# Kernel optimization log

Measured on AMD Instinct MI355X. Metric: run time of the kernel, lower is better.

Reference implementation:

```python
import math
import jax, jax.numpy as jnp
import numpy as np

T, D, H = 2048, 1024, 16
DH = D // H
DFF = 4 * D
EPS = 1e-5


def gelu(x):
    c = math.sqrt(2.0 / math.pi)
    return 0.5 * x * (1.0 + jnp.tanh(c * (x + 0.044715 * jnp.power(x, 3))))


def layer_norm(x, w, b):
    mu = jnp.mean(x, axis=-1, keepdims=True)
    var = jnp.var(x, axis=-1, keepdims=True)
    return (x - mu) / jnp.sqrt(var + EPS) * w + b


def setup_inputs() -> dict:
    key = jax.random.key(0)
    ks = jax.random.split(key, 8)
    s = lambda fan_in: 1.0 / math.sqrt(fan_in)
    return {
        "x": jax.random.normal(ks[0], (T, D), jnp.float32),
        "w_kqv": jax.random.uniform(ks[1], (3 * D, D), jnp.float32, -s(D), s(D)),
        "b_kqv": jnp.zeros((3 * D,), jnp.float32),
        "w_o": jax.random.uniform(ks[2], (D, D), jnp.float32, -s(D), s(D)),
        "b_o": jnp.zeros((D,), jnp.float32),
        "ln1_w": jnp.ones((D,), jnp.float32),
        "ln1_b": jnp.zeros((D,), jnp.float32),
        "ln2_w": jnp.ones((D,), jnp.float32),
        "ln2_b": jnp.zeros((D,), jnp.float32),
        "w_up": jax.random.uniform(ks[3], (DFF, D), jnp.float32, -s(D), s(D)),
        "b_up": jnp.zeros((DFF,), jnp.float32),
        "w_down": jax.random.uniform(ks[4], (D, DFF), jnp.float32, -s(DFF), s(DFF)),
        "b_down": jnp.zeros((D,), jnp.float32),
    }


def _block(x, w_kqv, b_kqv, w_o, b_o, ln1_w, ln1_b, ln2_w, ln2_b,
           w_up, b_up, w_down, b_down):
    t = x.shape[0]
    # --- causal attention ---
    h = layer_norm(x, ln1_w, ln1_b)
    kqv = h @ w_kqv.T + b_kqv                      # [t, 3D]
    k, q, v = jnp.split(kqv, 3, axis=-1)
    # rearrange 't (d h) -> h t d' : head index is the FAST axis (as in source)
    to_heads = lambda m: m.reshape(t, DH, H).transpose(2, 0, 1)  # [H, t, DH]
    k, q, v = to_heads(k), to_heads(q), to_heads(v)
    # NOTE: source divides by sqrt(1/d) == multiplies by sqrt(d_head)
    logits = jnp.einsum('hqd,hkd->hqk', q, k) * math.sqrt(DH)
    mask = jnp.tril(jnp.ones((t, t), dtype=bool))
    logits = jnp.where(mask, logits, -jnp.inf)
    attn_w = jax.nn.softmax(logits, axis=-1)       # [H, t, t]
    hv = jnp.einsum('hqK,hKd->hqd', attn_w, v)     # [H, t, DH]
    # rearrange 'h q d -> q (h d)' : head index is the SLOW axis (as in source)
    hv = hv.transpose(1, 0, 2).reshape(t, D)
    x = x + (hv @ w_o.T + b_o)
    # --- MLP ---
    h2 = layer_norm(x, ln2_w, ln2_b)
    z = gelu(h2 @ w_up.T + b_up) @ w_down.T + b_down
    return x + z


def reference(x, w_kqv, b_kqv, w_o, b_o, ln1_w, ln1_b, ln2_w, ln2_b,
              w_up, b_up, w_down, b_down):
    return _block(x, w_kqv, b_kqv, w_o, b_o, ln1_w, ln1_b, ln2_w, ln2_b,
                  w_up, b_up, w_down, b_down)
```

## Files before the change

### kernel.cpp

```cpp
#include <hip/hip_runtime.h>
#include <math.h>

#define TT 2048
#define DD 1024
#define NH 16
#define DHD 64
#define DFF 4096

typedef __attribute__((ext_vector_type(8))) short short8;
typedef __attribute__((ext_vector_type(4))) float f32x4;

#define MFMA16(a, b, c) __builtin_amdgcn_mfma_f32_16x16x32_bf16(a, b, c, 0, 0, 0)
#define GLDS16(gp, lp) __builtin_amdgcn_global_load_lds( \
    (const __attribute__((address_space(1))) void*)(gp), \
    (__attribute__((address_space(3))) void*)(lp), 16, 0, 0)

static __device__ __forceinline__ unsigned short f2b(float f) {
  unsigned u = __builtin_bit_cast(unsigned, f);
  u = u + 0x7fffu + ((u >> 16) & 1u);
  return (unsigned short)(u >> 16);
}
static __device__ __forceinline__ float b2f(unsigned short b) {
  return __builtin_bit_cast(float, (unsigned)b << 16);
}

__global__ __launch_bounds__(256) void f2b4_kernel(const float* __restrict__ s0,
    const float* __restrict__ s1, const float* __restrict__ s2,
    const float* __restrict__ s3, unsigned short* __restrict__ out) {
  int i = blockIdx.x * 256 + threadIdx.x;
  const float* s; int off;
  if (i < 786432)       { s = s0; off = 0; }
  else if (i < 1048576) { s = s1; off = 786432; }
  else if (i < 2097152) { s = s2; off = 1048576; }
  else                  { s = s3; off = 2097152; }
  float4 v = ((const float4*)s)[i - off];
  ushort4 o;
  o.x = f2b(v.x); o.y = f2b(v.y); o.z = f2b(v.z); o.w = f2b(v.w);
  ((ushort4*)out)[i] = o;
}

__global__ __launch_bounds__(256) void ln_kernel(const float* __restrict__ x,
    const float* __restrict__ w, const float* __restrict__ b,
    unsigned short* __restrict__ out) {
  int row = blockIdx.x;
  const float4* xr = (const float4*)(x + (size_t)row * DD);
  float4 v = xr[threadIdx.x];
  float s  = v.x + v.y + v.z + v.w;
  float ss = v.x * v.x + v.y * v.y + v.z * v.z + v.w * v.w;
  for (int o = 32; o > 0; o >>= 1) {
    s  += __shfl_down(s, o);
    ss += __shfl_down(ss, o);
  }
  __shared__ float red[10];
  int lane = threadIdx.x & 63, wv = threadIdx.x >> 6;
  if (lane == 0) { red[wv] = s; red[4 + wv] = ss; }
  __syncthreads();
  if (threadIdx.x == 0) {
    float S  = red[0] + red[1] + red[2] + red[3];
    float SS = red[4] + red[5] + red[6] + red[7];
    float mu  = S * (1.0f / DD);
    float var = SS * (1.0f / DD) - mu * mu;
    red[8] = mu;
    red[9] = rsqrtf(var + 1e-5f);
  }
  __syncthreads();
  float mu = red[8], inv = red[9];
  float4 wv4 = ((const float4*)w)[threadIdx.x];
  float4 bv4 = ((const float4*)b)[threadIdx.x];
  ushort4 o4;
  o4.x = f2b((v.x - mu) * inv * wv4.x + bv4.x);
  o4.y = f2b((v.y - mu) * inv * wv4.y + bv4.y);
  o4.z = f2b((v.z - mu) * inv * wv4.z + bv4.z);
  o4.w = f2b((v.w - mu) * inv * wv4.w + bv4.w);
  ((ushort4*)(out + (size_t)row * DD))[threadIdx.x] = o4;
}

template<int FUSE_GELU, int OUT_BF16, int HAS_RESID, int PARTIAL>
__global__ __launch_bounds__(256) void gemm3(
    const unsigned short* __restrict__ A,
    const unsigned short* __restrict__ Bw,
    const float* __restrict__ bias,
    const float* __restrict__ resid,
    void* __restrict__ Cout,
    int M, int N, int K, int KS) {
  __shared__ char lds[65536];
  const int tid = threadIdx.x;
  const int w = tid >> 6, l = tid & 63;
  const int l15 = l & 15, lhi = l >> 4;
  const int row0 = blockIdx.y * 128, col0 = blockIdx.x * 128;
  const int kbeg = blockIdx.z * KS;
  const int wm = (w >> 1) * 64, wn = (w & 1) * 64;

  f32x4 acc[4][4] = {};

  const int slotp = (l & 7) ^ (l >> 3);
  const int srow = w * 32 + 2 * (l >> 3) + (slotp >> 2);
  const int scolb = (slotp & 3) * 16;
  const char* aS = (const char*)A + ((size_t)(row0 + srow) * K + kbeg) * 2 + scolb;
  const char* bS = (const char*)Bw + ((size_t)(col0 + srow) * K + kbeg) * 2 + scolb;
  const size_t r16 = (size_t)K * 32;
  const int aLo = w * 2048;
  const int bLo = 8192 + w * 2048;

  int aOff[4], bOff[4];
#pragma unroll
  for (int i = 0; i < 4; ++i) {
    int ra = wm + i * 16 + l15;
    aOff[i] = (ra >> 1) * 128 + (((( ra & 1) << 6) | (lhi << 4)) ^ (((ra >> 1) & 7) << 4));
    int rb = wn + i * 16 + l15;
    bOff[i] = 8192 + (rb >> 1) * 128 + ((((rb & 1) << 6) | (lhi << 4)) ^ (((rb >> 1) & 7) << 4));
  }

  const int NT = KS >> 5;

  auto STAGE = [&](int t) {
    char* base = lds + (t & 3) * 16384;
    const char* a = aS + (size_t)t * 64;
    const char* b = bS + (size_t)t * 64;
    GLDS16(a, base + aLo);
    GLDS16(a + r16, base + aLo + 1024);
    GLDS16(b, base + bLo);
    GLDS16(b + r16, base + bLo + 1024);
  };
  auto COMPUTE = [&](int t) {
    const char* buf = lds + (t & 3) * 16384;
    short8 af[4], bf[4];
#pragma unroll
    for (int mi = 0; mi < 4; ++mi) af[mi] = *(const short8*)(buf + aOff[mi]);
#pragma unroll
    for (int ni = 0; ni < 4; ++ni) bf[ni] = *(const short8*)(buf + bOff[ni]);
#pragma unroll
    for (int mi = 0; mi < 4; ++mi)
#pragma unroll
      for (int ni = 0; ni < 4; ++ni)
        acc[mi][ni] = MFMA16(af[mi], bf[ni], acc[mi][ni]);
  };

  STAGE(0); STAGE(1); STAGE(2);

  int t = 0;
  for (; t < NT - 2; ++t) {
    __builtin_amdgcn_sched_barrier(0);
    asm volatile("s_waitcnt vmcnt(8)" ::: "memory");
    __builtin_amdgcn_s_barrier();
    __builtin_amdgcn_sched_barrier(0);
    if (t + 3 < NT) STAGE(t + 3);
    COMPUTE(t);
  }
  __builtin_amdgcn_sched_barrier(0);
  asm volatile("s_waitcnt vmcnt(4)" ::: "memory");
  __builtin_amdgcn_s_barrier();
  __builtin_amdgcn_sched_barrier(0);
  COMPUTE(NT - 2);
  __builtin_amdgcn_sched_barrier(0);
  asm volatile("s_waitcnt vmcnt(0)" ::: "memory");
  __builtin_amdgcn_s_barrier();
  __builtin_amdgcn_sched_barrier(0);
  COMPUTE(NT - 1);

  if (PARTIAL) {
    unsigned short* Cp = (unsigned short*)Cout + (size_t)blockIdx.z * M * N;
#pragma unroll
    for (int mi = 0; mi < 4; ++mi)
#pragma unroll
      for (int r = 0; r < 4; ++r) {
        size_t row = (size_t)(row0 + wm + mi * 16 + lhi * 4 + r);
#pragma unroll
        for (int ni = 0; ni < 4; ++ni)
          Cp[row * N + col0 + wn + ni * 16 + l15] = f2b(acc[mi][ni][r]);
      }
    return;
  }

#pragma unroll
  for (int mi = 0; mi < 4; ++mi) {
#pragma unroll
    for (int r = 0; r < 4; ++r) {
      size_t row = (size_t)(row0 + wm + mi * 16 + lhi * 4 + r);
#pragma unroll
      for (int ni = 0; ni < 4; ++ni) {
        int col = col0 + wn + ni * 16 + l15;
        float v = acc[mi][ni][r] + bias[col];
        if (FUSE_GELU) {
          float u = v;
          v = 0.5f * u * (1.0f + tanhf(0.7978845608028654f * (u + 0.044715f * u * u * u)));
        }
        if (HAS_RESID) v += resid[row * N + col];
        if (OUT_BF16) ((unsigned short*)Cout)[row * N + col] = f2b(v);
        else          ((float*)Cout)[row * N + col] = v;
      }
    }
  }
}

template<int NP>
__global__ __launch_bounds__(256) void reduce_k(const unsigned short* __restrict__ p,
    const float* __restrict__ bias, const float* __restrict__ resid,
    float* __restrict__ out) {
  int i = blockIdx.x * 256 + threadIdx.x;
  float4 r = ((const float4*)resid)[i];
  float4 bb = ((const float4*)bias)[i & (DD / 4 - 1)];
  float o0 = r.x + bb.x, o1 = r.y + bb.y, o2 = r.z + bb.z, o3 = r.w + bb.w;
#pragma unroll
  for (int z = 0; z < NP; ++z) {
    ushort4 pv = ((const ushort4*)(p + (size_t)z * TT * DD))[i];
    o0 += b2f(pv.x); o1 += b2f(pv.y); o2 += b2f(pv.z); o3 += b2f(pv.w);
  }
  float4 o; o.x = o0; o.y = o1; o.z = o2; o.w = o3;
  ((float4*)out)[i] = o;
}

__global__ __launch_bounds__(256) void gather_qkv(const unsigned short* __restrict__ kqv,
    unsigned short* __restrict__ Q, unsigned short* __restrict__ K) {
  int idx = blockIdx.x * 256 + threadIdx.x;
  int d = idx & 63;
  int t = (idx >> 6) & (TT - 1);
  int h = idx >> 17;
  int col = d * NH + h;
  const unsigned short* rowp = kqv + (size_t)t * (3 * DD);
  K[idx] = rowp[col];
  Q[idx] = f2b(b2f(rowp[DD + col]) * 8.0f);
}

__global__ __launch_bounds__(256) void transpose_v(const unsigned short* __restrict__ kqv,
    unsigned short* __restrict__ Vt) {
  const int h = blockIdx.y;
  const int t0 = blockIdx.x * 64;
  __shared__ unsigned short Vs[64][65];
  for (int idx = threadIdx.x; idx < 4096; idx += 256) {
    int t = idx >> 6, d = idx & 63;
    Vs[t][d] = kqv[(size_t)(t0 + t) * (3 * DD) + 2 * DD + d * NH + h];
  }
  __syncthreads();
  for (int idx = threadIdx.x; idx < 4096; idx += 256) {
    int d = idx >> 6, t = idx & 63;
    Vt[(size_t)(h * DHD + d) * TT + t0 + t] = Vs[t][d];
  }
}

__global__ __launch_bounds__(256) void attn_mfma(
    const unsigned short* __restrict__ Q,
    const unsigned short* __restrict__ K,
    const unsigned short* __restrict__ Vt,
    unsigned short* __restrict__ hv) {
  const int h = blockIdx.y;
  const int qb = gridDim.x - 1 - blockIdx.x;
  const int q0 = qb * 64;
  const int tid = threadIdx.x;
  const int w = tid >> 6, l = tid & 63;
  const int l15 = l & 15, lhi = l >> 4;

  __shared__ char lds[40960];
  char* Ps = lds + 32768 + w * 2048;

  const char* KhB = (const char*)(K + (size_t)h * TT * DHD);
  const char* VhB = (const char*)(Vt + (size_t)h * DHD * TT);

  const unsigned short* Qbase = Q + ((size_t)h * TT + q0 + w * 16 + l15) * DHD;
  short8 qf0 = *(const short8*)(Qbase + lhi * 8);
  short8 qf1 = *(const short8*)(Qbase + 32 + lhi * 8);

  f32x4 oacc[4] = {};
  float m = -1e30f, lsum = 0.0f;

  const int lrow = l >> 3;
  const int colb = ((l & 7) * 16) ^ (lrow << 4);
  const int srow = w * 16 + lrow;
  const int swz = (l15 & 7) << 4;

  auto stage = [&](int k0n, char* buf) {
    const char* ks = KhB + (size_t)(k0n + srow) * 128 + colb;
    GLDS16(ks, buf + w * 2048);
    GLDS16(ks + 8 * 128, buf + w * 2048 + 1024);
    const char* vs = VhB + (size_t)srow * (TT * 2) + (size_t)k0n * 2 + colb;
    GLDS16(vs, buf + 8192 + w * 2048);
    GLDS16(vs + 8 * (TT * 2), buf + 8192 + w * 2048 + 1024);
  };

  stage(0, lds);
  __syncthreads();
  int cur = 0;

  for (int kt = 0; kt <= qb; ++kt) {
    if (kt < qb) stage((kt + 1) * 64, lds + (cur ^ 1) * 16384);

    const char* Kb = lds + cur * 16384;
    const char* Vb = Kb + 8192;

    f32x4 sacc[4] = {};
    __builtin_amdgcn_s_setprio(1);
#pragma unroll
    for (int nt = 0; nt < 4; ++nt) {
      const char* rp = Kb + (nt * 16 + l15) * 128;
      short8 kb0 = *(const short8*)(rp + ((lhi * 16) ^ swz));
      short8 kb1 = *(const short8*)(rp + ((64 + lhi * 16) ^ swz));
      sacc[nt] = MFMA16(kb0, qf0, sacc[nt]);
      sacc[nt] = MFMA16(kb1, qf1, sacc[nt]);
    }
    __builtin_amdgcn_s_setprio(0);

    if (kt == qb) {
      const int qloc = w * 16 + l15;
#pragma unroll
      for (int nt = 0; nt < 4; ++nt)
#pragma unroll
        for (int r = 0; r < 4; ++r)
          if (nt * 16 + lhi * 4 + r > qloc) sacc[nt][r] = -1e30f;
    }

    float tmax = -1e30f;
#pragma unroll
    for (int nt = 0; nt < 4; ++nt)
#pragma unroll
      for (int r = 0; r < 4; ++r) tmax = fmaxf(tmax, sacc[nt][r]);
    tmax = fmaxf(tmax, __shfl_xor(tmax, 16));
    tmax = fmaxf(tmax, __shfl_xor(tmax, 32));
    float mnew = fmaxf(m, tmax);
    float al = __expf(m - mnew);
    m = mnew;
    float ssum = 0.0f;
#pragma unroll
    for (int nt = 0; nt < 4; ++nt)
#pragma unroll
      for (int r = 0; r < 4; ++r) {
        float p = __expf(sacc[nt][r] - mnew);
        sacc[nt][r] = p;
        ssum += p;
      }
    ssum += __shfl_xor(ssum, 16);
    ssum += __shfl_xor(ssum, 32);
    lsum = lsum * al + ssum;

    {
      char* pp = Ps + l15 * 128;
#pragma unroll
      for (int nt = 0; nt < 4; ++nt) {
        uint2 pk;
        pk.x = (unsigned)f2b(sacc[nt][0]) | ((unsigned)f2b(sacc[nt][1]) << 16);
        pk.y = (unsigned)f2b(sacc[nt][2]) | ((unsigned)f2b(sacc[nt][3]) << 16);
        *(uint2*)(pp + (((nt * 16 + lhi * 4) * 2) ^ swz)) = pk;
      }
    }

    float alr[4];
#pragma unroll
    for (int r = 0; r < 4; ++r) alr[r] = __shfl(al, (l & 48) | (lhi * 4 + r));
#pragma unroll
    for (int dt = 0; dt < 4; ++dt)
#pragma unroll
      for (int r = 0; r < 4; ++r) oacc[dt][r] *= alr[r];

    const char* pr = Ps + l15 * 128;
    short8 pa0 = *(const short8*)(pr + ((lhi * 16) ^ swz));
    short8 pa1 = *(const short8*)(pr + ((64 + lhi * 16) ^ swz));
    __builtin_amdgcn_s_setprio(1);
#pragma unroll
    for (int dt = 0; dt < 4; ++dt) {
      const char* vr = Vb + (dt * 16 + l15) * 128;
      short8 vb0 = *(const short8*)(vr + ((lhi * 16) ^ swz));
      short8 vb1 = *(const short8*)(vr + ((64 + lhi * 16) ^ swz));
      oacc[dt] = MFMA16(pa0, vb0, oacc[dt]);
      oacc[dt] = MFMA16(pa1, vb1, oacc[dt]);
    }
    __builtin_amdgcn_s_setprio(0);

    __syncthreads();
    cur ^= 1;
  }

  float lr[4];
#pragma unroll
  for (int r = 0; r < 4; ++r)
    lr[r] = 1.0f / __shfl(lsum, (l & 48) | (lhi * 4 + r));
#pragma unroll
  for (int r = 0; r < 4; ++r) {
    size_t orow = (size_t)(q0 + w * 16 + lhi * 4 + r) * DD + h * 64;
#pragma unroll
    for (int dt = 0; dt < 4; ++dt)
      hv[orow + dt * 16 + l15] = f2b(oacc[dt][r] * lr[r]);
  }
}

extern "C" void kernel_launch(void* const* d_in, const int* in_sizes, int n_in,
                              void* d_out, int out_size, void* d_ws, size_t ws_size,
                              hipStream_t stream) {
  const float* x     = (const float*)d_in[0];
  const float* w_kqv = (const float*)d_in[1];
  const float* b_kqv = (const float*)d_in[2];
  const float* w_o   = (const float*)d_in[3];
  const float* b_o   = (const float*)d_in[4];
  const float* ln1_w = (const float*)d_in[5];
  const float* ln1_b = (const float*)d_in[6];
  const float* ln2_w = (const float*)d_in[7];
  const float* ln2_b = (const float*)d_in[8];
  const float* w_up  = (const float*)d_in[9];
  const float* b_up  = (const float*)d_in[10];
  const float* w_dn  = (const float*)d_in[11];
  const float* b_dn  = (const float*)d_in[12];
  float* out = (float*)d_out;

  char* W = (char*)d_ws;
  unsigned short* wkqv_b = (unsigned short*)(W);
  unsigned short* wo_b   = (unsigned short*)(W + 6291456);
  unsigned short* wup_b  = (unsigned short*)(W + 8388608);
  unsigned short* wdn_b  = (unsigned short*)(W + 16777216);
  unsigned short* h_b    = (unsigned short*)(W + 25165824);
  unsigned short* kqz    = (unsigned short*)(W + 29360128);
  unsigned short* Qg     = (unsigned short*)(W + 46137344);
  unsigned short* Kg     = (unsigned short*)(W + 50331648);
  unsigned short* Vtg    = (unsigned short*)(W + 54525952);
  unsigned short* hv_b   = (unsigned short*)(W + 58720256);
  float*          x2     = (float*)(W + 62914560);
  unsigned short* pproj  = (unsigned short*)(W + 29360128);
  unsigned short* pdown  = (unsigned short*)(W + 46137344);

  f2b4_kernel<<<3145728 / 256, 256, 0, stream>>>(w_kqv, w_o, w_up, w_dn, wkqv_b);

  ln_kernel<<<TT, 256, 0, stream>>>(x, ln1_w, ln1_b, h_b);
  gemm3<0, 1, 0, 0><<<dim3(3 * DD / 128, TT / 128, 1), 256, 0, stream>>>(
      h_b, wkqv_b, b_kqv, nullptr, kqz, TT, 3 * DD, DD, DD);
  gather_qkv<<<(NH * TT * DHD) / 256, 256, 0, stream>>>(kqz, Qg, Kg);
  transpose_v<<<dim3(TT / 64, NH), 256, 0, stream>>>(kqz, Vtg);
  attn_mfma<<<dim3(TT / 64, NH), 256, 0, stream>>>(Qg, Kg, Vtg, hv_b);
  gemm3<0, 0, 0, 1><<<dim3(DD / 128, TT / 128, 2), 256, 0, stream>>>(
      hv_b, wo_b, nullptr, nullptr, pproj, TT, DD, DD, DD / 2);
  reduce_k<2><<<TT * DD / 4 / 256, 256, 0, stream>>>(pproj, b_o, x, x2);
  ln_kernel<<<TT, 256, 0, stream>>>(x2, ln2_w, ln2_b, h_b);
  gemm3<1, 1, 0, 0><<<dim3(DFF / 128, TT / 128, 1), 256, 0, stream>>>(
      h_b, wup_b, b_up, nullptr, kqz, TT, DFF, DD, DD);
  gemm3<0, 0, 0, 1><<<dim3(DD / 128, TT / 128, 4), 256, 0, stream>>>(
      kqz, wdn_b, nullptr, nullptr, pdown, TT, DD, DFF, DFF / 4);
  reduce_k<4><<<TT * DD / 4 / 256, 256, 0, stream>>>(pdown, b_dn, x2, out);
}
```

Baseline: 184.4 us.

## Remap GEMM and attention blocks per XCD and switch GEMM to BK=64 double buffering

GEMM blocks now come from a 1D grid and are remapped so that each of the 8 XCDs gets a contiguous CX×CY patch of output tiles, so blocks on the same XCD share A/B rows in L2. The GEMM K-step grows from 32 to 64 with two 32 KB LDS buffers instead of four 16 KB ones, using a simpler row-swizzled layout. The attention grid is likewise remapped so each XCD handles two heads, and its initial __syncthreads is replaced with explicit vmcnt waits plus barriers. Pipeline depth drops from three stages in flight to one prefetch, which may expose more load latency.

```diff
diff --git a/kernel.cpp b/kernel.cpp
--- a/kernel.cpp
+++ b/kernel.cpp
@@ -76,90 +76,88 @@
 }
 
 template<int FUSE_GELU, int OUT_BF16, int HAS_RESID, int PARTIAL>
-__global__ __launch_bounds__(256) void gemm3(
+__global__ __launch_bounds__(256) void gemm4(
     const unsigned short* __restrict__ A,
     const unsigned short* __restrict__ Bw,
     const float* __restrict__ bias,
     const float* __restrict__ resid,
     void* __restrict__ Cout,
-    int M, int N, int K, int KS) {
+    int M, int N, int K, int KS, int CX, int CY) {
   __shared__ char lds[65536];
   const int tid = threadIdx.x;
   const int w = tid >> 6, l = tid & 63;
   const int l15 = l & 15, lhi = l >> 4;
-  const int row0 = blockIdx.y * 128, col0 = blockIdx.x * 128;
-  const int kbeg = blockIdx.z * KS;
+
+  const int GX = N >> 7, GYM = M >> 7;
+  const int xcd = blockIdx.x & 7, s = blockIdx.x >> 3;
+  const int ncx = GX / CX;
+  const int bx = (xcd % ncx) * CX + (s % CX);
+  const int yz = (xcd / ncx) * CY + (s / CX);
+  const int by = yz % GYM, bz = yz / GYM;
+
+  const int row0 = by << 7, col0 = bx << 7;
+  const int kbeg = bz * KS;
   const int wm = (w >> 1) * 64, wn = (w & 1) * 64;
 
   f32x4 acc[4][4] = {};
 
-  const int slotp = (l & 7) ^ (l >> 3);
-  const int srow = w * 32 + 2 * (l >> 3) + (slotp >> 2);
-  const int scolb = (slotp & 3) * 16;
-  const char* aS = (const char*)A + ((size_t)(row0 + srow) * K + kbeg) * 2 + scolb;
-  const char* bS = (const char*)Bw + ((size_t)(col0 + srow) * K + kbeg) * 2 + scolb;
-  const size_t r16 = (size_t)K * 32;
-  const int aLo = w * 2048;
-  const int bLo = 8192 + w * 2048;
-
-  int aOff[4], bOff[4];
-#pragma unroll
-  for (int i = 0; i < 4; ++i) {
-    int ra = wm + i * 16 + l15;
-    aOff[i] = (ra >> 1) * 128 + (((( ra & 1) << 6) | (lhi << 4)) ^ (((ra >> 1) & 7) << 4));
-    int rb = wn + i * 16 + l15;
-    bOff[i] = 8192 + (rb >> 1) * 128 + ((((rb & 1) << 6) | (lhi << 4)) ^ (((rb >> 1) & 7) << 4));
-  }
-
-  const int NT = KS >> 5;
+  const int lr = l >> 3;
+  const int cb = ((l & 7) * 16) ^ (lr << 4);
+  const char* aS = (const char*)A + ((size_t)(row0 + w * 32 + lr) * K + kbeg) * 2 + cb;
+  const char* bS = (const char*)Bw + ((size_t)(col0 + w * 32 + lr) * K + kbeg) * 2 + cb;
+  const size_t r8 = (size_t)K * 16;
+  const int aO = w * 4096, bO = 16384 + w * 4096;
+  const int NT = KS >> 6;
 
   auto STAGE = [&](int t) {
-    char* base = lds + (t & 3) * 16384;
-    const char* a = aS + (size_t)t * 64;
-    const char* b = bS + (size_t)t * 64;
-    GLDS16(a, base + aLo);
-    GLDS16(a + r16, base + aLo + 1024);
-    GLDS16(b, base + bLo);
-    GLDS16(b + r16, base + bLo + 1024);
+    char* base = lds + (t & 1) * 32768;
+    const char* a = aS + (size_t)t * 128;
+    const char* b = bS + (size_t)t * 128;
+    GLDS16(a,            base + aO);
+    GLDS16(a +     r8,   base + aO + 1024);
+    GLDS16(a + 2 * r8,   base + aO + 2048);
+    GLDS16(a + 3 * r8,   base + aO + 3072);
+    GLDS16(b,            base + bO);
+    GLDS16(b +     r8,   base + bO + 1024);
+    GLDS16(b + 2 * r8,   base + bO + 2048);
+    GLDS16(b + 3 * r8,   base + bO + 3072);
   };
   auto COMPUTE = [&](int t) {
-    const char* buf = lds + (t & 3) * 16384;
-    short8 af[4], bf[4];
-#pragma unroll
-    for (int mi = 0; mi < 4; ++mi) af[mi] = *(const short8*)(buf + aOff[mi]);
-#pragma unroll
-    for (int ni = 0; ni < 4; ++ni) bf[ni] = *(const short8*)(buf + bOff[ni]);
-#pragma unroll
-    for (int mi = 0; mi < 4; ++mi)
+    const char* Ab = lds + (t & 1) * 32768;
+    const char* Bb = Ab + 16384;
+    const int sw = (l15 & 7) << 4;
+#pragma unroll
+    for (int kk = 0; kk < 2; ++kk) {
+      short8 af[4], bf[4];
+#pragma unroll
+      for (int mi = 0; mi < 4; ++mi)
+        af[mi] = *(const short8*)(Ab + (wm + mi * 16 + l15) * 128 + ((kk * 64 + lhi * 16) ^ sw));
 #pragma unroll
       for (int ni = 0; ni < 4; ++ni)
-        acc[mi][ni] = MFMA16(af[mi], bf[ni], acc[mi][ni]);
+        bf[ni] = *(const short8*)(Bb + (wn + ni * 16 + l15) * 128 + ((kk * 64 + lhi * 16) ^ sw));
+#pragma unroll
+      for (int mi = 0; mi < 4; ++mi)
+#pragma unroll
+        for (int ni = 0; ni < 4; ++ni)
+          acc[mi][ni] = MFMA16(af[mi], bf[ni], acc[mi][ni]);
+    }
   };
 
-  STAGE(0); STAGE(1); STAGE(2);
-
-  int t = 0;
-  for (; t < NT - 2; ++t) {
-    __builtin_amdgcn_sched_barrier(0);
-    asm volatile("s_waitcnt vmcnt(8)" ::: "memory");
+  STAGE(0);
+  for (int t = 0; t < NT; ++t) {
+    if (t + 1 < NT) STAGE(t + 1);
+    __builtin_amdgcn_sched_barrier(0);
+    if (t + 1 < NT) asm volatile("s_waitcnt vmcnt(8)" ::: "memory");
+    else            asm volatile("s_waitcnt vmcnt(0)" ::: "memory");
     __builtin_amdgcn_s_barrier();
     __builtin_amdgcn_sched_barrier(0);
-    if (t + 3 < NT) STAGE(t + 3);
     COMPUTE(t);
-  }
-  __builtin_amdgcn_sched_barrier(0);
-  asm volatile("s_waitcnt vmcnt(4)" ::: "memory");
-  __builtin_amdgcn_s_barrier();
-  __builtin_amdgcn_sched_barrier(0);
-  COMPUTE(NT - 2);
-  __builtin_amdgcn_sched_barrier(0);
-  asm volatile("s_waitcnt vmcnt(0)" ::: "memory");
-  __builtin_amdgcn_s_barrier();
-  __builtin_amdgcn_sched_barrier(0);
-  COMPUTE(NT - 1);
+    __builtin_amdgcn_sched_barrier(0);
+    __builtin_amdgcn_s_barrier();
+  }
 
   if (PARTIAL) {
-    unsigned short* Cp = (unsigned short*)Cout + (size_t)blockIdx.z * M * N;
+    unsigned short* Cp = (unsigned short*)Cout + (size_t)bz * M * N;
 #pragma unroll
     for (int mi = 0; mi < 4; ++mi)
 #pragma unroll
@@ -243,8 +241,10 @@
     const unsigned short* __restrict__ K,
     const unsigned short* __restrict__ Vt,
     unsigned short* __restrict__ hv) {
-  const int h = blockIdx.y;
-  const int qb = gridDim.x - 1 - blockIdx.x;
+  const int bid = blockIdx.x;
+  const int xcd = bid & 7, s = bid >> 3;
+  const int qb = 31 - (s & 31);
+  const int h  = xcd * 2 + (s >> 5);
   const int q0 = qb * 64;
   const int tid = threadIdx.x;
   const int w = tid >> 6, l = tid & 63;
@@ -263,9 +263,9 @@
   f32x4 oacc[4] = {};
   float m = -1e30f, lsum = 0.0f;
 
-  const int lrow = l >> 3;
-  const int colb = ((l & 7) * 16) ^ (lrow << 4);
-  const int srow = w * 16 + lrow;
+  const int lr = l >> 3;
+  const int colb = ((l & 7) * 16) ^ (lr << 4);
+  const int srow = w * 16 + lr;
   const int swz = (l15 & 7) << 4;
 
   auto stage = [&](int k0n, char* buf) {
@@ -278,11 +278,15 @@
   };
 
   stage(0, lds);
-  __syncthreads();
   int cur = 0;
 
   for (int kt = 0; kt <= qb; ++kt) {
     if (kt < qb) stage((kt + 1) * 64, lds + (cur ^ 1) * 16384);
+    __builtin_amdgcn_sched_barrier(0);
+    if (kt < qb) asm volatile("s_waitcnt vmcnt(4)" ::: "memory");
+    else         asm volatile("s_waitcnt vmcnt(0)" ::: "memory");
+    __builtin_amdgcn_s_barrier();
+    __builtin_amdgcn_sched_barrier(0);
 
     const char* Kb = lds + cur * 16384;
     const char* Vb = Kb + 8192;
@@ -364,20 +368,21 @@
     }
     __builtin_amdgcn_s_setprio(0);
 
-    __syncthreads();
+    __builtin_amdgcn_sched_barrier(0);
+    __builtin_amdgcn_s_barrier();
     cur ^= 1;
   }
 
-  float lr[4];
+  float lr4[4];
 #pragma unroll
   for (int r = 0; r < 4; ++r)
-    lr[r] = 1.0f / __shfl(lsum, (l & 48) | (lhi * 4 + r));
+    lr4[r] = 1.0f / __shfl(lsum, (l & 48) | (lhi * 4 + r));
 #pragma unroll
   for (int r = 0; r < 4; ++r) {
     size_t orow = (size_t)(q0 + w * 16 + lhi * 4 + r) * DD + h * 64;
 #pragma unroll
     for (int dt = 0; dt < 4; ++dt)
-      hv[orow + dt * 16 + l15] = f2b(oacc[dt][r] * lr[r]);
+      hv[orow + dt * 16 + l15] = f2b(oacc[dt][r] * lr4[r]);
   }
 }
 
@@ -417,18 +422,18 @@
   f2b4_kernel<<<3145728 / 256, 256, 0, stream>>>(w_kqv, w_o, w_up, w_dn, wkqv_b);
 
   ln_kernel<<<TT, 256, 0, stream>>>(x, ln1_w, ln1_b, h_b);
-  gemm3<0, 1, 0, 0><<<dim3(3 * DD / 128, TT / 128, 1), 256, 0, stream>>>(
-      h_b, wkqv_b, b_kqv, nullptr, kqz, TT, 3 * DD, DD, DD);
+  gemm4<0, 1, 0, 0><<<384, 256, 0, stream>>>(
+      h_b, wkqv_b, b_kqv, nullptr, kqz, TT, 3 * DD, DD, DD, 6, 8);
   gather_qkv<<<(NH * TT * DHD) / 256, 256, 0, stream>>>(kqz, Qg, Kg);
   transpose_v<<<dim3(TT / 64, NH), 256, 0, stream>>>(kqz, Vtg);
-  attn_mfma<<<dim3(TT / 64, NH), 256, 0, stream>>>(Qg, Kg, Vtg, hv_b);
-  gemm3<0, 0, 0, 1><<<dim3(DD / 128, TT / 128, 2), 256, 0, stream>>>(
-      hv_b, wo_b, nullptr, nullptr, pproj, TT, DD, DD, DD / 2);
+  attn_mfma<<<512, 256, 0, stream>>>(Qg, Kg, Vtg, hv_b);
+  gemm4<0, 0, 0, 1><<<256, 256, 0, stream>>>(
+      hv_b, wo_b, nullptr, nullptr, pproj, TT, DD, DD, DD / 2, 8, 4);
   reduce_k<2><<<TT * DD / 4 / 256, 256, 0, stream>>>(pproj, b_o, x, x2);
   ln_kernel<<<TT, 256, 0, stream>>>(x2, ln2_w, ln2_b, h_b);
-  gemm3<1, 1, 0, 0><<<dim3(DFF / 128, TT / 128, 1), 256, 0, stream>>>(
-      h_b, wup_b, b_up, nullptr, kqz, TT, DFF, DD, DD);
-  gemm3<0, 0, 0, 1><<<dim3(DD / 128, TT / 128, 4), 256, 0, stream>>>(
-      kqz, wdn_b, nullptr, nullptr, pdown, TT, DD, DFF, DFF / 4);
+  gemm4<1, 1, 0, 0><<<512, 256, 0, stream>>>(
+      h_b, wup_b, b_up, nullptr, kqz, TT, DFF, DD, DD, 8, 8);
+  gemm4<0, 0, 0, 1><<<512, 256, 0, stream>>>(
+      kqz, wdn_b, nullptr, nullptr, pdown, TT, DD, DFF, DFF / 4, 8, 8);
   reduce_k<4><<<TT * DD / 4 / 256, 256, 0, stream>>>(pdown, b_dn, x2, out);
 }
```

After: 171.4 us. 7.0% less time.
